# Kernel optimization log

Hardware: AMD Instinct MI355X
Metric: run time of the kernel (lower is better)

## Reference

```python
import jax, jax.numpy as jnp
import numpy as np

T = 20.0  # temperature
SCALE = 0.3

def reference(outputs1, outputs2, outputs3, outputs4, outputs5, outputs6, outputs7, outputs8, targets):
    # preds: [M=8, B, C] tempered softmaxes
    logits = jnp.stack([outputs1, outputs2, outputs3, outputs4,
                        outputs5, outputs6, outputs7, outputs8], axis=0)
    preds = jax.nn.softmax(logits / T, axis=-1)
    # center over class dim (Pearson correlation per sample per model)
    v = preds - jnp.mean(preds, axis=-1, keepdims=True)
    v = v / jnp.sqrt(jnp.sum(v * v, axis=-1, keepdims=True))  # unit-norm rows
    # Gram over model pairs: [B, M, M]
    G = jnp.einsum('mbc,nbc->bmn', v, v)
    M = G.shape[-1]
    # sum over upper triangle (j<k); diagonal entries are exactly 1 pre-normalization
    d = (jnp.sum(G, axis=(1, 2)) - jnp.trace(G, axis1=1, axis2=2)) * 0.5  # [B]
    loss = SCALE * d
    return jnp.mean(loss)

def setup_inputs() -> dict:
    key = jax.random.key(0)
    ks = jax.random.split(key, 9)
    B, C = 4096, 1000
    inp = {f'outputs{i+1}': jax.random.normal(ks[i], (B, C), dtype=jnp.float32)
           for i in range(8)}
    inp['targets'] = jax.random.randint(ks[8], (B,), 0, C, dtype=jnp.int64)
    return inp
```

## Files before the change

### kernel.cpp

```cpp
#include <hip/hip_runtime.h>
#include <math.h>


constexpr int NC   = 1000;
constexpr int NC4  = 250;
constexpr int NM   = 8;
constexpr float TINV = 1.0f / 20.0f;
constexpr float INVC = 1.0f / (float)NC;

__device__ __forceinline__ float waveMax(float v) {
#pragma unroll
    for (int o = 32; o > 0; o >>= 1) v = fmaxf(v, __shfl_xor(v, o, 64));
    return v;
}
__device__ __forceinline__ float waveSum(float v) {
#pragma unroll
    for (int o = 32; o > 0; o >>= 1) v += __shfl_xor(v, o, 64);
    return v;
}
__device__ __forceinline__ double waveSumD(double v) {
#pragma unroll
    for (int o = 32; o > 0; o >>= 1) v += __shfl_xor(v, o, 64);
    return v;
}

__global__ __launch_bounds__(64, 2) void div8_main(
    const float* __restrict__ in0, const float* __restrict__ in1,
    const float* __restrict__ in2, const float* __restrict__ in3,
    const float* __restrict__ in4, const float* __restrict__ in5,
    const float* __restrict__ in6, const float* __restrict__ in7,
    float* __restrict__ part)
{
    const int b    = blockIdx.x;
    const int lane = threadIdx.x;
    const bool act3 = lane < (NC4 - 3 * 64);

    const float* rows[NM] = {
        in0 + (size_t)b * NC, in1 + (size_t)b * NC,
        in2 + (size_t)b * NC, in3 + (size_t)b * NC,
        in4 + (size_t)b * NC, in5 + (size_t)b * NC,
        in6 + (size_t)b * NC, in7 + (size_t)b * NC };

    float4 x[NM][4];
#pragma unroll
    for (int m = 0; m < NM; ++m) {
        const float4* p = reinterpret_cast<const float4*>(rows[m]);
#pragma unroll
        for (int j = 0; j < 4; ++j) {
            if (j < 3)
                x[m][j] = p[lane + 64 * j];
            else
                x[m][j] = act3 ? p[lane + 192]
                               : make_float4(-INFINITY, -INFINITY, -INFINITY, -INFINITY);
        }
    }

    float mxs[NM];
#pragma unroll
    for (int m = 0; m < NM; ++m) {
        float v = fmaxf(fmaxf(x[m][0].x, x[m][0].y), fmaxf(x[m][0].z, x[m][0].w));
#pragma unroll
        for (int j = 1; j < 4; ++j)
            v = fmaxf(v, fmaxf(fmaxf(x[m][j].x, x[m][j].y),
                               fmaxf(x[m][j].z, x[m][j].w)));
        mxs[m] = waveMax(v) * TINV;
    }

    float invS[NM];
#pragma unroll
    for (int m = 0; m < NM; ++m) {
        float s = 0.f;
#pragma unroll
        for (int j = 0; j < 4; ++j) {
            x[m][j].x = __expf(fmaf(x[m][j].x, TINV, -mxs[m]));
            x[m][j].y = __expf(fmaf(x[m][j].y, TINV, -mxs[m]));
            x[m][j].z = __expf(fmaf(x[m][j].z, TINV, -mxs[m]));
            x[m][j].w = __expf(fmaf(x[m][j].w, TINV, -mxs[m]));
            s += (x[m][j].x + x[m][j].y) + (x[m][j].z + x[m][j].w);
        }
        invS[m] = 1.0f / waveSum(s);
    }

    float am[NM], bm[NM];
#pragma unroll
    for (int m = 0; m < NM; ++m) {
        float qq = 0.f;
#pragma unroll
        for (int j = 0; j < 4; ++j) {
            if (j == 3 && !act3) continue;
            float u0 = fmaf(x[m][j].x, invS[m], -INVC);
            float u1 = fmaf(x[m][j].y, invS[m], -INVC);
            float u2 = fmaf(x[m][j].z, invS[m], -INVC);
            float u3 = fmaf(x[m][j].w, invS[m], -INVC);
            qq = fmaf(u0, u0, fmaf(u1, u1, fmaf(u2, u2, fmaf(u3, u3, qq))));
        }
        float qt = waveSum(qq);
        float rm = 1.0f / sqrtf(qt);
        am[m] = invS[m] * rm;
        bm[m] = -INVC * rm;
    }

    double cr = 0.0;
#pragma unroll
    for (int j = 0; j < 4; ++j) {
        if (j == 3 && !act3) continue;
        float tx = 0.f, ty = 0.f, tz = 0.f, tw = 0.f;
        float sx = 0.f, sy = 0.f, sz = 0.f, sw = 0.f;
#pragma unroll
        for (int m = 0; m < NM; ++m) {
            float wx_ = fmaf(x[m][j].x, am[m], bm[m]); tx += wx_; sx = fmaf(wx_, wx_, sx);
            float wy_ = fmaf(x[m][j].y, am[m], bm[m]); ty += wy_; sy = fmaf(wy_, wy_, sy);
            float wz_ = fmaf(x[m][j].z, am[m], bm[m]); tz += wz_; sz = fmaf(wz_, wz_, sz);
            float ww_ = fmaf(x[m][j].w, am[m], bm[m]); tw += ww_; sw = fmaf(ww_, ww_, sw);
        }
        cr += (double)fmaf(tx, tx, -sx);
        cr += (double)fmaf(ty, ty, -sy);
        cr += (double)fmaf(tz, tz, -sz);
        cr += (double)fmaf(tw, tw, -sw);
    }
    cr = waveSumD(cr);
    if (lane == 0) part[b] = (float)cr;
}

__global__ __launch_bounds__(256) void div8_final(
    const float* __restrict__ part, float* __restrict__ out, int B)
{
    const int t = threadIdx.x;
    double acc = 0.0;
    for (int i = t; i < B; i += 256) acc += (double)part[i];
    acc = waveSumD(acc);
    __shared__ double redd[4];
    if ((t & 63) == 0) redd[t >> 6] = acc;
    __syncthreads();
    if (t == 0) {
        double tot = (redd[0] + redd[1]) + (redd[2] + redd[3]);
        out[0] = (float)(tot * (0.5 * 0.3 / (double)B));
    }
}

extern "C" void kernel_launch(void* const* d_in, const int* in_sizes, int n_in,
                              void* d_out, int out_size, void* d_ws, size_t ws_size,
                              hipStream_t stream)
{
    const float* a0 = (const float*)d_in[0];
    const float* a1 = (const float*)d_in[1];
    const float* a2 = (const float*)d_in[2];
    const float* a3 = (const float*)d_in[3];
    const float* a4 = (const float*)d_in[4];
    const float* a5 = (const float*)d_in[5];
    const float* a6 = (const float*)d_in[6];
    const float* a7 = (const float*)d_in[7];
    const int B = in_sizes[0] / NC;

    float* part = (float*)d_ws;

    div8_main<<<B, 64, 0, stream>>>(a0, a1, a2, a3, a4, a5, a6, a7, part);
    div8_final<<<1, 256, 0, stream>>>(part, (float*)d_out, B);
}
```

Before: 35.98 us.

## Stream models one at a time, drop max-subtraction, pack four rows per block

Each of the eight model rows is now processed fully (exp, sum, centering norm, accumulation into running t and s vectors) before the next is loaded, instead of holding all 32 float4 per lane at once. The max reduction is removed, relying on logits/20 staying small enough that exp cannot overflow. The normalization is rewritten to use unnormalized exps with a scaled mean, and blocks now carry four waves (one row each). This cuts register pressure, one wave reduction per model, and an exp-argument fma, in exchange for less memory-level parallelism per wave and reliance on the input range.

After: 36.73 us. +2.1%, slower.

```diff
diff --git a/kernel.cpp b/kernel.cpp
--- a/kernel.cpp
+++ b/kernel.cpp
@@ -8,11 +8,6 @@
 constexpr float TINV = 1.0f / 20.0f;
 constexpr float INVC = 1.0f / (float)NC;
 
-__device__ __forceinline__ float waveMax(float v) {
-#pragma unroll
-    for (int o = 32; o > 0; o >>= 1) v = fmaxf(v, __shfl_xor(v, o, 64));
-    return v;
-}
 __device__ __forceinline__ float waveSum(float v) {
 #pragma unroll
     for (int o = 32; o > 0; o >>= 1) v += __shfl_xor(v, o, 64);
@@ -24,15 +19,17 @@
     return v;
 }
 
-__global__ __launch_bounds__(64, 2) void div8_main(
+__global__ __launch_bounds__(256, 4) void div8_main(
     const float* __restrict__ in0, const float* __restrict__ in1,
     const float* __restrict__ in2, const float* __restrict__ in3,
     const float* __restrict__ in4, const float* __restrict__ in5,
     const float* __restrict__ in6, const float* __restrict__ in7,
-    float* __restrict__ part)
+    float* __restrict__ part, int B)
 {
-    const int b    = blockIdx.x;
-    const int lane = threadIdx.x;
+    const int wid  = threadIdx.x >> 6;
+    const int lane = threadIdx.x & 63;
+    const int b    = blockIdx.x * 4 + wid;
+    if (b >= B) return;
     const bool act3 = lane < (NC4 - 3 * 64);
 
     const float* rows[NM] = {
@@ -41,82 +38,68 @@
         in4 + (size_t)b * NC, in5 + (size_t)b * NC,
         in6 + (size_t)b * NC, in7 + (size_t)b * NC };
 
-    float4 x[NM][4];
+    float4 t4[4], s4[4];
+#pragma unroll
+    for (int j = 0; j < 4; ++j) {
+        t4[j] = make_float4(0.f, 0.f, 0.f, 0.f);
+        s4[j] = make_float4(0.f, 0.f, 0.f, 0.f);
+    }
+
 #pragma unroll
     for (int m = 0; m < NM; ++m) {
         const float4* p = reinterpret_cast<const float4*>(rows[m]);
+
+        float4 e[4];
 #pragma unroll
         for (int j = 0; j < 4; ++j) {
-            if (j < 3)
-                x[m][j] = p[lane + 64 * j];
-            else
-                x[m][j] = act3 ? p[lane + 192]
-                               : make_float4(-INFINITY, -INFINITY, -INFINITY, -INFINITY);
+            float4 v = (j < 3) ? p[lane + 64 * j]
+                     : (act3 ? p[lane + 192]
+                             : make_float4(-INFINITY, -INFINITY, -INFINITY, -INFINITY));
+            e[j].x = __expf(v.x * TINV);
+            e[j].y = __expf(v.y * TINV);
+            e[j].z = __expf(v.z * TINV);
+            e[j].w = __expf(v.w * TINV);
         }
-    }
 
-    float mxs[NM];
-#pragma unroll
-    for (int m = 0; m < NM; ++m) {
-        float v = fmaxf(fmaxf(x[m][0].x, x[m][0].y), fmaxf(x[m][0].z, x[m][0].w));
-#pragma unroll
-        for (int j = 1; j < 4; ++j)
-            v = fmaxf(v, fmaxf(fmaxf(x[m][j].x, x[m][j].y),
-                               fmaxf(x[m][j].z, x[m][j].w)));
-        mxs[m] = waveMax(v) * TINV;
-    }
-
-    float invS[NM];
-#pragma unroll
-    for (int m = 0; m < NM; ++m) {
         float s = 0.f;
 #pragma unroll
-        for (int j = 0; j < 4; ++j) {
-            x[m][j].x = __expf(fmaf(x[m][j].x, TINV, -mxs[m]));
-            x[m][j].y = __expf(fmaf(x[m][j].y, TINV, -mxs[m]));
-            x[m][j].z = __expf(fmaf(x[m][j].z, TINV, -mxs[m]));
-            x[m][j].w = __expf(fmaf(x[m][j].w, TINV, -mxs[m]));
-            s += (x[m][j].x + x[m][j].y) + (x[m][j].z + x[m][j].w);
-        }
-        invS[m] = 1.0f / waveSum(s);
-    }
+        for (int j = 0; j < 4; ++j)
+            s += (e[j].x + e[j].y) + (e[j].z + e[j].w);
+        const float S  = waveSum(s);
+        const float SC = S * INVC;
 
-    float am[NM], bm[NM];
-#pragma unroll
-    for (int m = 0; m < NM; ++m) {
         float qq = 0.f;
 #pragma unroll
         for (int j = 0; j < 4; ++j) {
             if (j == 3 && !act3) continue;
-            float u0 = fmaf(x[m][j].x, invS[m], -INVC);
-            float u1 = fmaf(x[m][j].y, invS[m], -INVC);
-            float u2 = fmaf(x[m][j].z, invS[m], -INVC);
-            float u3 = fmaf(x[m][j].w, invS[m], -INVC);
+            float u0 = e[j].x - SC;
+            float u1 = e[j].y - SC;
+            float u2 = e[j].z - SC;
+            float u3 = e[j].w - SC;
             qq = fmaf(u0, u0, fmaf(u1, u1, fmaf(u2, u2, fmaf(u3, u3, qq))));
         }
-        float qt = waveSum(qq);
-        float rm = 1.0f / sqrtf(qt);
-        am[m] = invS[m] * rm;
-        bm[m] = -INVC * rm;
+        const float qt = waveSum(qq);
+        const float rm = 1.0f / sqrtf(qt);
+        const float bmv = -SC * rm;
+
+#pragma unroll
+        for (int j = 0; j < 4; ++j) {
+            if (j == 3 && !act3) continue;
+            float w;
+            w = fmaf(e[j].x, rm, bmv); t4[j].x += w; s4[j].x = fmaf(w, w, s4[j].x);
+            w = fmaf(e[j].y, rm, bmv); t4[j].y += w; s4[j].y = fmaf(w, w, s4[j].y);
+            w = fmaf(e[j].z, rm, bmv); t4[j].z += w; s4[j].z = fmaf(w, w, s4[j].z);
+            w = fmaf(e[j].w, rm, bmv); t4[j].w += w; s4[j].w = fmaf(w, w, s4[j].w);
+        }
     }
 
     double cr = 0.0;
 #pragma unroll
     for (int j = 0; j < 4; ++j) {
-        if (j == 3 && !act3) continue;
-        float tx = 0.f, ty = 0.f, tz = 0.f, tw = 0.f;
-        float sx = 0.f, sy = 0.f, sz = 0.f, sw = 0.f;
-#pragma unroll
-        for (int m = 0; m < NM; ++m) {
-            float wx_ = fmaf(x[m][j].x, am[m], bm[m]); tx += wx_; sx = fmaf(wx_, wx_, sx);
-            float wy_ = fmaf(x[m][j].y, am[m], bm[m]); ty += wy_; sy = fmaf(wy_, wy_, sy);
-            float wz_ = fmaf(x[m][j].z, am[m], bm[m]); tz += wz_; sz = fmaf(wz_, wz_, sz);
-            float ww_ = fmaf(x[m][j].w, am[m], bm[m]); tw += ww_; sw = fmaf(ww_, ww_, sw);
-        }
-        cr += (double)fmaf(tx, tx, -sx);
-        cr += (double)fmaf(ty, ty, -sy);
-        cr += (double)fmaf(tz, tz, -sz);
-        cr += (double)fmaf(tw, tw, -sw);
+        cr += (double)fmaf(t4[j].x, t4[j].x, -s4[j].x);
+        cr += (double)fmaf(t4[j].y, t4[j].y, -s4[j].y);
+        cr += (double)fmaf(t4[j].z, t4[j].z, -s4[j].z);
+        cr += (double)fmaf(t4[j].w, t4[j].w, -s4[j].w);
     }
     cr = waveSumD(cr);
     if (lane == 0) part[b] = (float)cr;
@@ -154,6 +137,7 @@
 
     float* part = (float*)d_ws;
 
-    div8_main<<<B, 64, 0, stream>>>(a0, a1, a2, a3, a4, a5, a6, a7, part);
+    const int grid = (B + 3) / 4;
+    div8_main<<<grid, 256, 0, stream>>>(a0, a1, a2, a3, a4, a5, a6, a7, part, B);
     div8_final<<<1, 256, 0, stream>>>(part, (float*)d_out, B);
 }
```
